# Performance work log

Measured on AMD Instinct MI355X. Metric: run time of the kernel, lower is better.

The kernel has to match this reference:

```python
import jax, jax.numpy as jnp
import numpy as np

N_GT, N_NODES, N_SPECIES, N_EDGES, D, L = 512, 399, 200, 397, 64, 2


def setup_inputs() -> dict:
    rng = np.random.default_rng(0)
    # Random recursive trees: parent of node i is uniform in [0, i).
    par = (rng.random((N_GT, N_NODES - 1)) * np.arange(1, N_NODES)).astype(np.int64)
    child = np.broadcast_to(np.arange(1, N_NODES), (N_GT, N_NODES - 1))
    off = (np.arange(N_GT, dtype=np.int64) * N_NODES)[:, None]
    c = (child + off).ravel()
    p = (par + off).ravel()
    # Both directions, as in the original [2, 2E_gt] convention.
    edge_index = np.stack([np.concatenate([c, p]), np.concatenate([p, c])])
    sp = np.full(N_NODES, -1, dtype=np.int64)
    sp[:N_SPECIES] = np.arange(N_SPECIES)
    sp_ids = np.tile(sp, N_GT)
    leaf_mask = sp_ids >= 0
    batch_vec = np.repeat(np.arange(N_GT, dtype=np.int64), N_NODES)
    # Clades: random species subsets per species-tree edge, guaranteed nonempty.
    pe = rng.uniform(0.05, 0.5, (N_EDGES, 1))
    clade_mask = rng.random((N_EDGES, N_SPECIES)) < pe
    clade_mask[np.arange(N_EDGES), rng.integers(0, N_SPECIES, N_EDGES)] = True
    key = jax.random.key(0)
    ks = jax.random.split(key, 3)
    s = 1.0 / np.sqrt(D)
    return {
        "edge_index": jnp.asarray(edge_index),
        "sp_ids": jnp.asarray(sp_ids),
        "leaf_mask": jnp.asarray(leaf_mask),
        "batch_vec": jnp.asarray(batch_vec),
        "clade_mask": jnp.asarray(clade_mask),
        "n_gt": N_GT,
        "emb_table": jax.random.normal(ks[0], (N_SPECIES + 1, D), jnp.float32),
        "W1": jax.random.normal(ks[1], (L, D, D), jnp.float32) * s,
        "b1": jnp.zeros((L, D), jnp.float32),
        "W2": jax.random.normal(ks[2], (L, D, D), jnp.float32) * s,
        "b2": jnp.zeros((L, D), jnp.float32),
        "eps": jnp.zeros((L,), jnp.float32),  # GINConv train_eps init 0
        "ln_gamma": jnp.ones((L, D), jnp.float32),
        "ln_beta": jnp.zeros((L, D), jnp.float32),
    }


def _layernorm(x, g, b):
    mu = x.mean(-1, keepdims=True)
    var = ((x - mu) ** 2).mean(-1, keepdims=True)
    return (x - mu) * jax.lax.rsqrt(var + 1e-5) * g + b


def reference(edge_index, sp_ids, leaf_mask, batch_vec, clade_mask, n_gt,
              emb_table, W1, b1, W2, b2, eps, ln_gamma, ln_beta):
    n_nodes = sp_ids.shape[0]
    n_edges, n_species = clade_mask.shape
    d = emb_table.shape[1]
    # Species embedding (internal nodes -> extra row n_species).
    emb_ids = jnp.where(sp_ids < 0, n_species, sp_ids)
    x = emb_table[emb_ids]  # [Nn, D]
    src, dst = edge_index[0], edge_index[1]
    for l in range(W1.shape[0]):
        # GINConv: mlp((1+eps)*x + sum_neighbors x_j), residual, LayerNorm.
        msg = jax.ops.segment_sum(x[src], dst, num_segments=n_nodes)
        h = (1.0 + eps[l]) * x + msg
        h = jax.nn.relu(h @ W1[l] + b1[l]) @ W2[l] + b2[l]
        x = _layernorm(x + h, ln_gamma[l], ln_beta[l])
        # dropout is identity in eval mode
    # Species pooling: mean over valid leaves per (gene tree, species).
    w = (leaf_mask & (sp_ids >= 0)).astype(x.dtype)  # [Nn]
    comp = batch_vec * n_species + jnp.maximum(sp_ids, 0)
    pool_size = n_gt * n_species
    sums = jax.ops.segment_sum(x * w[:, None], comp, num_segments=pool_size)
    cnts = jax.ops.segment_sum(w, comp, num_segments=pool_size)
    pool = (sums / jnp.maximum(cnts, 1.0)[:, None]).reshape(n_gt, n_species, d)
    valid = (cnts > 0).astype(x.dtype).reshape(n_gt, n_species)  # [G, S]
    # Clade pooling per species-tree edge (vectorized over the per-edge loop).
    mf = clade_mask.astype(x.dtype)  # [E, S]
    csum = jnp.einsum('es,gsd->egd', mf, pool * valid[:, :, None])  # [E,G,D]
    ccnt = mf @ valid.T  # [E, G] valid-species count per (edge, gene tree)
    gt_means = csum / jnp.maximum(ccnt, 1.0)[:, :, None]
    has = (ccnt > 0).astype(x.dtype)  # gene trees with data for this edge
    n_v = has.sum(1)  # [E]
    mean = (gt_means * has[:, :, None]).sum(1) / jnp.maximum(n_v, 1.0)[:, None]
    diff = (gt_means - mean[:, None, :]) * has[:, :, None]
    var = (diff ** 2).sum(1) / jnp.maximum(n_v - 1.0, 1.0)[:, None]  # unbiased
    ok = (n_v > 1)[:, None]
    std = jnp.where(ok, jnp.sqrt(jnp.where(ok, var, 1.0)), 0.0)
    mean = jnp.where((n_v > 0)[:, None], mean, 0.0)
    return jnp.concatenate([mean, std], axis=-1)  # [n_edges, 2*D]
```

## Files before the change

kernel.cpp:

```cpp
#include <hip/hip_runtime.h>

#define SMAX 200
#define NPG 399

typedef __bf16 bf16x8 __attribute__((ext_vector_type(8)));
typedef _Float16 half8 __attribute__((ext_vector_type(8)));
typedef float f32x4 __attribute__((ext_vector_type(4)));

__device__ __forceinline__ unsigned short f2bf(float f) {
  unsigned u = __float_as_uint(f);
  unsigned r = (u + 0x7FFFu + ((u >> 16) & 1u)) >> 16;
  return (unsigned short)r;
}
__device__ __forceinline__ int xel(int node, int dim) {
  return node * 64 + ((((dim >> 3)) ^ (node & 7)) << 3) + (dim & 7);
}

__global__ __launch_bounds__(256) void k_prep(const int* __restrict__ clade,
                                              unsigned short* __restrict__ mfA,
                                              unsigned* __restrict__ mfbits,
                                              int n_edges, int n_species) {
  int stride = gridDim.x * 256;
  for (int idx = blockIdx.x * 256 + threadIdx.x; idx < 25 * 7 * 512;
       idx += stride) {
    int fi = idx >> 9, within = idx & 511;
    int mt = fi / 7, kt = fi % 7;
    int l = within >> 3, j = within & 7;
    int e = mt * 16 + (l & 15);
    int s = kt * 32 + ((l >> 4) & 3) * 8 + j;
    unsigned short v = 0;
    if (e < n_edges && s < n_species && clade[(size_t)e * n_species + s] != 0)
      v = 0x3F80;
    mfA[idx] = v;
  }
  for (int idx = blockIdx.x * 256 + threadIdx.x; idx < 400 * 8; idx += stride) {
    int e = idx >> 3, w = idx & 7;
    unsigned bits = 0;
    if (e < n_edges && w < 7) {
      for (int b = 0; b < 32; ++b) {
        int s = w * 32 + b;
        if (s < n_species && clade[(size_t)e * n_species + s] != 0)
          bits |= 1u << b;
      }
    }
    mfbits[idx] = bits;
  }
}

__global__ __launch_bounds__(512) void k_tree(
    const float* __restrict__ emb, const int* __restrict__ sp,
    const int* __restrict__ leaf, const int* __restrict__ src,
    const int* __restrict__ dst, const float* __restrict__ W1,
    const float* __restrict__ b1, const float* __restrict__ W2,
    const float* __restrict__ b2, const float* __restrict__ eps_p,
    const float* __restrict__ gam, const float* __restrict__ bet,
    const unsigned short* __restrict__ mfA, const unsigned* __restrict__ mfbits,
    float* __restrict__ gmat, float* __restrict__ has, int npg, int n_species,
    int n_edges, int n_gt) {
  __shared__ __attribute__((aligned(16))) _Float16 sA[NPG * 64];
  __shared__ __attribute__((aligned(16))) _Float16 sB[NPG * 64];
  __shared__ __attribute__((aligned(16))) _Float16 sWf[2][2][4096];
  __shared__ __attribute__((aligned(16))) _Float16 sT[8][1024];
  __shared__ int sStart[NPG + 1];
  __shared__ int sChild[NPG - 1];
  __shared__ int sPar[NPG];
  __shared__ int sCnt[NPG];

  int g = blockIdx.x, tid = threadIdx.x;
  int base = g * npg, nEt = npg - 1, ebase = g * nEt;
  int w = tid >> 6, lane = tid & 63;
  int cc = lane & 15, gq = lane >> 4;

  for (int i = tid; i < npg + 1; i += 512) sStart[i] = 0;
  for (int i = tid; i < npg; i += 512) sCnt[i] = 0;
  __syncthreads();
  for (int idx = tid; idx < 4096; idx += 512) {
    int k = idx >> 6, n = idx & 63;
    int frag = (k >> 5) * 4 + (n >> 4);
    int ln = ((k >> 3) & 3) * 16 + (n & 15);
    int j = k & 7;
    int o = frag * 512 + ln * 8 + j;
    sWf[0][0][o] = (_Float16)W1[idx];
    sWf[0][1][o] = (_Float16)W2[idx];
    sWf[1][0][o] = (_Float16)W1[4096 + idx];
    sWf[1][1][o] = (_Float16)W2[4096 + idx];
  }
  for (int idx = tid; idx < npg * 8; idx += 512) {
    int node = idx >> 3, ch = idx & 7;
    int s = sp[base + node];
    int row = (s < 0) ? n_species : s;
    float4 v0 = reinterpret_cast<const float4*>(emb)[row * 16 + ch * 2];
    float4 v1 = reinterpret_cast<const float4*>(emb)[row * 16 + ch * 2 + 1];
    half8 h;
    h[0] = (_Float16)v0.x; h[1] = (_Float16)v0.y;
    h[2] = (_Float16)v0.z; h[3] = (_Float16)v0.w;
    h[4] = (_Float16)v1.x; h[5] = (_Float16)v1.y;
    h[6] = (_Float16)v1.z; h[7] = (_Float16)v1.w;
    *reinterpret_cast<half8*>(&sA[node * 64 + ((ch ^ (node & 7)) << 3)]) = h;
  }
  for (int i = tid; i < nEt; i += 512) {
    int c = src[ebase + i] - base;
    int p = dst[ebase + i] - base;
    sPar[c] = p;
    atomicAdd(&sStart[p + 1], 1);
  }
  __syncthreads();
  if (w == 0) {
    int run = 0;
    for (int chunk = 0; chunk * 64 < npg + 1; ++chunk) {
      int idx = chunk * 64 + lane;
      int v = (idx < npg + 1) ? sStart[idx] : 0;
      for (int off = 1; off < 64; off <<= 1) {
        int t2 = __shfl_up(v, off);
        if (lane >= off) v += t2;
      }
      v += run;
      if (idx < npg + 1) sStart[idx] = v;
      run = __shfl(v, 63);
    }
  }
  __syncthreads();
  for (int c = tid + 1; c < npg; c += 512) {
    int p = sPar[c];
    int pos = sStart[p] + atomicAdd(&sCnt[p], 1);
    sChild[pos] = c;
  }
  __syncthreads();

  _Float16* tb = sT[w];
  for (int l = 0; l < 2; ++l) {
    const _Float16* xin = l ? sB : sA;
    _Float16* xout = l ? sA : sB;
    const half8* xin8 = reinterpret_cast<const half8*>(xin);
    float e1 = 1.0f + eps_p[l];
    float b1v[4], b2v[4], gv[4], bv[4];
#pragma unroll
    for (int nt = 0; nt < 4; ++nt) {
      b1v[nt] = b1[l * 64 + cc + 16 * nt];
      b2v[nt] = b2[l * 64 + cc + 16 * nt];
      gv[nt] = gam[l * 64 + cc + 16 * nt];
      bv[nt] = bet[l * 64 + cc + 16 * nt];
    }
    const half8* B1 = reinterpret_cast<const half8*>(sWf[l][0]);
    const half8* B2 = reinterpret_cast<const half8*>(sWf[l][1]);
    for (int t = w; t < 25; t += 8) {
      int n0 = t * 16;
      int node = n0 + cc;
      bool vn = node < npg;
      int nd2 = vn ? node : 0;
      int j = vn ? sStart[nd2] : 0;
      int e = vn ? sStart[nd2 + 1] : 0;
      half8 s0 = xin8[nd2 * 8 + (gq ^ (nd2 & 7))];
      half8 s1 = xin8[nd2 * 8 + ((4 + gq) ^ (nd2 & 7))];
      bool hasp = vn && node > 0;
      int pr = hasp ? sPar[nd2] : 0;
      half8 p0 = xin8[pr * 8 + (gq ^ (pr & 7))];
      half8 p1 = xin8[pr * 8 + ((4 + gq) ^ (pr & 7))];
      float a0f[8], a1f[8];
#pragma unroll
      for (int d = 0; d < 8; ++d) {
        a0f[d] = e1 * (float)s0[d] + (hasp ? (float)p0[d] : 0.f);
        a1f[d] = e1 * (float)s1[d] + (hasp ? (float)p1[d] : 0.f);
      }
      while (__any(j < e)) {
        bool act = j < e;
        int c = act ? sChild[j] : 0;
        half8 v0 = xin8[c * 8 + (gq ^ (c & 7))];
        half8 v1 = xin8[c * 8 + ((4 + gq) ^ (c & 7))];
        if (act) {
#pragma unroll
          for (int d = 0; d < 8; ++d) {
            a0f[d] += (float)v0[d];
            a1f[d] += (float)v1[d];
          }
          ++j;
        }
      }
      half8 a0, a1;
#pragma unroll
      for (int d = 0; d < 8; ++d) {
        a0[d] = (_Float16)a0f[d];
        a1[d] = (_Float16)a1f[d];
      }
      f32x4 tacc[4];
#pragma unroll
      for (int nt = 0; nt < 4; ++nt) tacc[nt] = (f32x4){0.f, 0.f, 0.f, 0.f};
#pragma unroll
      for (int nt = 0; nt < 4; ++nt) {
        tacc[nt] = __builtin_amdgcn_mfma_f32_16x16x32_f16(
            a0, B1[nt * 64 + lane], tacc[nt], 0, 0, 0);
        tacc[nt] = __builtin_amdgcn_mfma_f32_16x16x32_f16(
            a1, B1[(4 + nt) * 64 + lane], tacc[nt], 0, 0, 0);
      }
#pragma unroll
      for (int nt = 0; nt < 4; ++nt)
#pragma unroll
        for (int r = 0; r < 4; ++r) {
          int m = gq * 4 + r;
          tb[m * 64 + ((cc + 16 * nt) ^ ((m & 7) << 3))] =
              (_Float16)fmaxf(tacc[nt][r] + b1v[nt], 0.f);
        }
      int sw = (cc & 7) << 3;
      half8 c0 =
          *reinterpret_cast<const half8*>(&tb[cc * 64 + ((gq * 8) ^ sw)]);
      half8 c1 =
          *reinterpret_cast<const half8*>(&tb[cc * 64 + ((32 + gq * 8) ^ sw)]);
      f32x4 hacc[4];
#pragma unroll
      for (int nt = 0; nt < 4; ++nt) hacc[nt] = (f32x4){0.f, 0.f, 0.f, 0.f};
#pragma unroll
      for (int nt = 0; nt < 4; ++nt) {
        hacc[nt] = __builtin_amdgcn_mfma_f32_16x16x32_f16(
            c0, B2[nt * 64 + lane], hacc[nt], 0, 0, 0);
        hacc[nt] = __builtin_amdgcn_mfma_f32_16x16x32_f16(
            c1, B2[(4 + nt) * 64 + lane], hacc[nt], 0, 0, 0);
      }
      float y[4][4];
#pragma unroll
      for (int r = 0; r < 4; ++r) {
        int nd3 = n0 + gq * 4 + r;
        bool v3 = nd3 < npg;
        int nds = v3 ? nd3 : 0;
#pragma unroll
        for (int nt = 0; nt < 4; ++nt) {
          float xv = (float)xin[xel(nds, cc + 16 * nt)];
          y[r][nt] = (v3 ? xv : 0.f) + hacc[nt][r] + b2v[nt];
        }
      }
#pragma unroll
      for (int r = 0; r < 4; ++r) {
        float s = y[r][0] + y[r][1] + y[r][2] + y[r][3];
        s += __shfl_xor(s, 1);
        s += __shfl_xor(s, 2);
        s += __shfl_xor(s, 4);
        s += __shfl_xor(s, 8);
        float mu = s * (1.f / 64.f);
        float d0 = y[r][0] - mu, d1 = y[r][1] - mu;
        float d2 = y[r][2] - mu, d3 = y[r][3] - mu;
        float v = d0 * d0 + d1 * d1 + d2 * d2 + d3 * d3;
        v += __shfl_xor(v, 1);
        v += __shfl_xor(v, 2);
        v += __shfl_xor(v, 4);
        v += __shfl_xor(v, 8);
        float iv = rsqrtf(v * (1.f / 64.f) + 1e-5f);
        int nd3 = n0 + gq * 4 + r;
        if (nd3 < npg) {
#pragma unroll
          for (int nt = 0; nt < 4; ++nt)
            xout[xel(nd3, cc + 16 * nt)] =
                (_Float16)((y[r][nt] - mu) * iv * gv[nt] + bv[nt]);
        }
      }
    }
    __syncthreads();
  }

  unsigned short* sBfU = reinterpret_cast<unsigned short*>(&sWf[0][0][0]);
  char* aux = reinterpret_cast<char*>(&sT[0][0]);
  float* sInv = reinterpret_cast<float*>(aux);
  float* sHas = reinterpret_cast<float*>(aux + 1600);
  unsigned* svb = reinterpret_cast<unsigned*>(aux + 3200);
  for (int i = tid; i < n_species + 1; i += 512) sStart[i] = 0;
  for (int i = tid; i < n_species; i += 512) sCnt[i] = 0;
  __syncthreads();
  for (int i = tid; i < npg; i += 512) {
    int s = sp[base + i];
    if (s >= 0 && leaf[base + i] != 0) atomicAdd(&sStart[s + 1], 1);
  }
  __syncthreads();
  if (w == 0) {
    int run = 0;
    for (int chunk = 0; chunk * 64 < n_species + 1; ++chunk) {
      int idx = chunk * 64 + lane;
      int v = (idx < n_species + 1) ? sStart[idx] : 0;
      for (int off = 1; off < 64; off <<= 1) {
        int t2 = __shfl_up(v, off);
        if (lane >= off) v += t2;
      }
      v += run;
      if (idx < n_species + 1) sStart[idx] = v;
      run = __shfl(v, 63);
    }
  }
  __syncthreads();
  for (int i = tid; i < npg; i += 512) {
    int s = sp[base + i];
    if (s >= 0 && leaf[base + i] != 0) {
      int pos = sStart[s] + atomicAdd(&sCnt[s], 1);
      sPar[pos] = i;
    }
  }
  __syncthreads();
  for (int idx = tid; idx < 14336; idx += 512) {
    int frag = idx >> 9;
    int ln = (idx >> 3) & 63;
    int jj = idx & 7;
    int s = (frag >> 2) * 32 + ((ln >> 4) & 3) * 8 + jj;
    int d = (frag & 3) * 16 + (ln & 15);
    float v = 0.f;
    if (s < n_species) {
      int j0 = sStart[s], j1 = sStart[s + 1];
      float sum = 0.f;
      for (int j2 = j0; j2 < j1; ++j2) {
        int nd4 = sPar[j2];
        sum += (float)sA[xel(nd4, d)];
      }
      if (j1 > j0) v = sum / (float)(j1 - j0);
    }
    sBfU[idx] = f2bf(v);
  }
  if (tid < 7) {
    unsigned bits = 0;
    for (int b = 0; b < 32; ++b) {
      int s = tid * 32 + b;
      if (s < n_species && sStart[s + 1] > sStart[s]) bits |= 1u << b;
    }
    svb[tid] = bits;
  }
  __syncthreads();
  for (int e = tid; e < 400; e += 512) {
    unsigned ccv = 0;
#pragma unroll
    for (int w2 = 0; w2 < 7; ++w2) ccv += __popc(mfbits[e * 8 + w2] & svb[w2]);
    sInv[e] = 1.f / (float)max(ccv, 1u);
    sHas[e] = (ccv > 0) ? 1.f : 0.f;
  }
  __syncthreads();
  const bf16x8* A = reinterpret_cast<const bf16x8*>(mfA);
  const bf16x8* Bb = reinterpret_cast<const bf16x8*>(sBfU);
  for (int mt = w; mt < 25; mt += 8) {
    bf16x8 af[7];
#pragma unroll
    for (int kt = 0; kt < 7; ++kt) af[kt] = A[(mt * 7 + kt) * 64 + lane];
    f32x4 acc0 = {0.f, 0.f, 0.f, 0.f};
    f32x4 acc1 = {0.f, 0.f, 0.f, 0.f};
    f32x4 acc2 = {0.f, 0.f, 0.f, 0.f};
    f32x4 acc3 = {0.f, 0.f, 0.f, 0.f};
#pragma unroll
    for (int kt = 0; kt < 7; ++kt) {
      const bf16x8* B = Bb + kt * 256 + lane;
      acc0 = __builtin_amdgcn_mfma_f32_16x16x32_bf16(af[kt], B[0], acc0, 0, 0, 0);
      acc1 = __builtin_amdgcn_mfma_f32_16x16x32_bf16(af[kt], B[64], acc1, 0, 0, 0);
      acc2 = __builtin_amdgcn_mfma_f32_16x16x32_bf16(af[kt], B[128], acc2, 0, 0, 0);
      acc3 = __builtin_amdgcn_mfma_f32_16x16x32_bf16(af[kt], B[192], acc3, 0, 0, 0);
    }
    int rbase = mt * 16 + (lane >> 4) * 4;
    int col = lane & 15;
#pragma unroll
    for (int r = 0; r < 4; ++r) {
      int e = rbase + r;
      if (e >= n_edges) continue;
      float inv = sInv[e];
      float* gp = gmat + ((size_t)e * n_gt + g) * 64 + col;
      gp[0] = acc0[r] * inv;
      gp[16] = acc1[r] * inv;
      gp[32] = acc2[r] * inv;
      gp[48] = acc3[r] * inv;
      if (col == 0) has[(size_t)e * n_gt + g] = sHas[e];
    }
  }
}

__global__ __launch_bounds__(512) void k_stat(const float* __restrict__ gmat,
                                              const float* __restrict__ has,
                                              float* __restrict__ out,
                                              int n_gt) {
  __shared__ float red1[8][64];
  __shared__ float red2[8][64];
  __shared__ float redn[8];
  int e = blockIdx.x;
  int tid = threadIdx.x, w = tid >> 6, lane = tid & 63;
  const float* ge = gmat + (size_t)e * n_gt * 64;
  const float* he = has + (size_t)e * n_gt;
  float S1 = 0.f, S2 = 0.f, nv = 0.f;
  for (int g = w; g < n_gt; g += 8) {
    float h = he[g];
    float v = ge[g * 64 + lane];
    S1 += h * v;
    S2 += h * v * v;
    nv += h;
  }
  red1[w][lane] = S1;
  red2[w][lane] = S2;
  if (lane == 0) redn[w] = nv;
  __syncthreads();
  if (w == 0) {
    float s1 = 0.f, s2 = 0.f, n_v = 0.f;
#pragma unroll
    for (int j = 0; j < 8; ++j) {
      s1 += red1[j][lane];
      s2 += red2[j][lane];
      n_v += redn[j];
    }
    float mean = s1 / fmaxf(n_v, 1.f);
    float var = (s2 - s1 * s1 / fmaxf(n_v, 1.f)) / fmaxf(n_v - 1.f, 1.f);
    float stdv = (n_v > 1.f) ? sqrtf(fmaxf(var, 0.f)) : 0.f;
    out[(size_t)e * 128 + lane] = (n_v > 0.f) ? mean : 0.f;
    out[(size_t)e * 128 + 64 + lane] = stdv;
  }
}

extern "C" void kernel_launch(void* const* d_in, const int* in_sizes, int n_in,
                              void* d_out, int out_size, void* d_ws, size_t ws_size,
                              hipStream_t stream) {
  (void)n_in; (void)out_size; (void)ws_size;
  const int* edge_index = (const int*)d_in[0];
  const int* sp_ids = (const int*)d_in[1];
  const int* leaf_mask = (const int*)d_in[2];
  const int* clade_mask = (const int*)d_in[4];
  const float* emb = (const float*)d_in[6];
  const float* W1 = (const float*)d_in[7];
  const float* b1 = (const float*)d_in[8];
  const float* W2 = (const float*)d_in[9];
  const float* b2 = (const float*)d_in[10];
  const float* eps = (const float*)d_in[11];
  const float* lng = (const float*)d_in[12];
  const float* lnb = (const float*)d_in[13];
  float* out = (float*)d_out;

  const int n_nodes = in_sizes[1];
  const int nE = in_sizes[0] / 2;
  const int n_species = in_sizes[6] / 64 - 1;
  const int n_edges = in_sizes[4] / n_species;
  const int n_gt = 512;
  const int npg = n_nodes / n_gt;

  const int* src = edge_index;
  const int* dst = edge_index + nE;

  float* gmat = (float*)d_ws;
  size_t gsz = ((size_t)n_edges * n_gt * 64 * sizeof(float) + 255ul) & ~255ul;
  float* has = (float*)((char*)d_ws + gsz);
  size_t hsz = ((size_t)n_edges * n_gt * sizeof(float) + 255ul) & ~255ul;
  unsigned short* mfA = (unsigned short*)((char*)d_ws + gsz + hsz);
  size_t masz = ((size_t)25 * 7 * 512 * sizeof(unsigned short) + 255ul) & ~255ul;
  unsigned* mfbits = (unsigned*)((char*)d_ws + gsz + hsz + masz);

  k_prep<<<64, 256, 0, stream>>>(clade_mask, mfA, mfbits, n_edges, n_species);
  k_tree<<<n_gt, 512, 0, stream>>>(emb, sp_ids, leaf_mask, src, dst, W1, b1,
                                   W2, b2, eps, lng, lnb, mfA, mfbits, gmat,
                                   has, npg, n_species, n_edges, n_gt);
  k_stat<<<n_edges, 512, 0, stream>>>(gmat, has, out, n_gt);
}
```

Before: 135.0 us.

## Store per-tree clade means in fp16 and restructure tree aggregation loops

The intermediate gmat buffer (edges x gene trees x 64) is now written and read as fp16 instead of fp32, halving the global traffic between k_tree and k_stat. The GIN neighbor loop now runs to a wave-uniform maximum child count instead of re-testing __any each step, and tiles are split into contiguous per-wave ranges. Species pooling now gathers 8 dims per thread with vector LDS loads instead of one scalar per thread, after zero-filling the bf16 buffer. The fp16 intermediate costs precision in the mean and std statistics, and the last wave takes four tiles while the others take three.

Result: faster. 123.0 us (-8.9%).

```diff
diff --git a/kernel.cpp b/kernel.cpp
--- a/kernel.cpp
+++ b/kernel.cpp
@@ -55,8 +55,8 @@
     const float* __restrict__ b2, const float* __restrict__ eps_p,
     const float* __restrict__ gam, const float* __restrict__ bet,
     const unsigned short* __restrict__ mfA, const unsigned* __restrict__ mfbits,
-    float* __restrict__ gmat, float* __restrict__ has, int npg, int n_species,
-    int n_edges, int n_gt) {
+    _Float16* __restrict__ gmat, float* __restrict__ has, int npg,
+    int n_species, int n_edges, int n_gt) {
   __shared__ __attribute__((aligned(16))) _Float16 sA[NPG * 64];
   __shared__ __attribute__((aligned(16))) _Float16 sB[NPG * 64];
   __shared__ __attribute__((aligned(16))) _Float16 sWf[2][2][4096];
@@ -128,6 +128,8 @@
   __syncthreads();
 
   _Float16* tb = sT[w];
+  int t0w = w * 3;
+  int t1w = (w == 7) ? 25 : t0w + 3;
   for (int l = 0; l < 2; ++l) {
     const _Float16* xin = l ? sB : sA;
     _Float16* xout = l ? sA : sB;
@@ -143,13 +145,13 @@
     }
     const half8* B1 = reinterpret_cast<const half8*>(sWf[l][0]);
     const half8* B2 = reinterpret_cast<const half8*>(sWf[l][1]);
-    for (int t = w; t < 25; t += 8) {
+    for (int t = t0w; t < t1w; ++t) {
       int n0 = t * 16;
       int node = n0 + cc;
       bool vn = node < npg;
       int nd2 = vn ? node : 0;
-      int j = vn ? sStart[nd2] : 0;
-      int e = vn ? sStart[nd2 + 1] : 0;
+      int j0v = vn ? sStart[nd2] : 0;
+      int cnt = vn ? (sStart[nd2 + 1] - j0v) : 0;
       half8 s0 = xin8[nd2 * 8 + (gq ^ (nd2 & 7))];
       half8 s1 = xin8[nd2 * 8 + ((4 + gq) ^ (nd2 & 7))];
       bool hasp = vn && node > 0;
@@ -162,9 +164,16 @@
         a0f[d] = e1 * (float)s0[d] + (hasp ? (float)p0[d] : 0.f);
         a1f[d] = e1 * (float)s1[d] + (hasp ? (float)p1[d] : 0.f);
       }
-      while (__any(j < e)) {
-        bool act = j < e;
-        int c = act ? sChild[j] : 0;
+      int cmax = cnt;
+#pragma unroll
+      for (int off = 1; off < 64; off <<= 1)
+        cmax = max(cmax, __shfl_xor(cmax, off));
+      cmax = __builtin_amdgcn_readfirstlane(cmax);
+#pragma unroll 2
+      for (int k = 0; k < cmax; ++k) {
+        bool act = k < cnt;
+        int jidx = act ? (j0v + k) : 0;
+        int c = sChild[jidx];
         half8 v0 = xin8[c * 8 + (gq ^ (c & 7))];
         half8 v1 = xin8[c * 8 + ((4 + gq) ^ (c & 7))];
         if (act) {
@@ -173,7 +182,6 @@
             a0f[d] += (float)v0[d];
             a1f[d] += (float)v1[d];
           }
-          ++j;
         }
       }
       half8 a0, a1;
@@ -262,6 +270,11 @@
   unsigned* svb = reinterpret_cast<unsigned*>(aux + 3200);
   for (int i = tid; i < n_species + 1; i += 512) sStart[i] = 0;
   for (int i = tid; i < n_species; i += 512) sCnt[i] = 0;
+  {
+    float4 z4 = {0.f, 0.f, 0.f, 0.f};
+    for (int i = tid; i < 1792; i += 512)
+      reinterpret_cast<float4*>(sBfU)[i] = z4;
+  }
   __syncthreads();
   for (int i = tid; i < npg; i += 512) {
     int s = sp[base + i];
@@ -291,23 +304,25 @@
     }
   }
   __syncthreads();
-  for (int idx = tid; idx < 14336; idx += 512) {
-    int frag = idx >> 9;
-    int ln = (idx >> 3) & 63;
-    int jj = idx & 7;
-    int s = (frag >> 2) * 32 + ((ln >> 4) & 3) * 8 + jj;
-    int d = (frag & 3) * 16 + (ln & 15);
-    float v = 0.f;
-    if (s < n_species) {
-      int j0 = sStart[s], j1 = sStart[s + 1];
-      float sum = 0.f;
-      for (int j2 = j0; j2 < j1; ++j2) {
-        int nd4 = sPar[j2];
-        sum += (float)sA[xel(nd4, d)];
-      }
-      if (j1 > j0) v = sum / (float)(j1 - j0);
-    }
-    sBfU[idx] = f2bf(v);
+  for (int idx = tid; idx < n_species * 8; idx += 512) {
+    int s = idx >> 3, dc = idx & 7;
+    int j0 = sStart[s], j1 = sStart[s + 1];
+    float sum[8] = {0.f, 0.f, 0.f, 0.f, 0.f, 0.f, 0.f, 0.f};
+    for (int j2 = j0; j2 < j1; ++j2) {
+      int nd = sPar[j2];
+      half8 v = *reinterpret_cast<const half8*>(
+          &sA[nd * 64 + ((dc ^ (nd & 7)) << 3)]);
+#pragma unroll
+      for (int dd = 0; dd < 8; ++dd) sum[dd] += (float)v[dd];
+    }
+    float invc = (j1 > j0) ? 1.f / (float)(j1 - j0) : 0.f;
+#pragma unroll
+    for (int dd = 0; dd < 8; ++dd) {
+      int d = dc * 8 + dd;
+      int frag = (s >> 5) * 4 + (d >> 4);
+      int ln = ((s >> 3) & 3) * 16 + (d & 15);
+      sBfU[frag * 512 + ln * 8 + (s & 7)] = f2bf(sum[dd] * invc);
+    }
   }
   if (tid < 7) {
     unsigned bits = 0;
@@ -351,17 +366,17 @@
       int e = rbase + r;
       if (e >= n_edges) continue;
       float inv = sInv[e];
-      float* gp = gmat + ((size_t)e * n_gt + g) * 64 + col;
-      gp[0] = acc0[r] * inv;
-      gp[16] = acc1[r] * inv;
-      gp[32] = acc2[r] * inv;
-      gp[48] = acc3[r] * inv;
+      _Float16* gp = gmat + ((size_t)e * n_gt + g) * 64 + col;
+      gp[0] = (_Float16)(acc0[r] * inv);
+      gp[16] = (_Float16)(acc1[r] * inv);
+      gp[32] = (_Float16)(acc2[r] * inv);
+      gp[48] = (_Float16)(acc3[r] * inv);
       if (col == 0) has[(size_t)e * n_gt + g] = sHas[e];
     }
   }
 }
 
-__global__ __launch_bounds__(512) void k_stat(const float* __restrict__ gmat,
+__global__ __launch_bounds__(512) void k_stat(const _Float16* __restrict__ gmat,
                                               const float* __restrict__ has,
                                               float* __restrict__ out,
                                               int n_gt) {
@@ -370,12 +385,12 @@
   __shared__ float redn[8];
   int e = blockIdx.x;
   int tid = threadIdx.x, w = tid >> 6, lane = tid & 63;
-  const float* ge = gmat + (size_t)e * n_gt * 64;
+  const _Float16* ge = gmat + (size_t)e * n_gt * 64;
   const float* he = has + (size_t)e * n_gt;
   float S1 = 0.f, S2 = 0.f, nv = 0.f;
   for (int g = w; g < n_gt; g += 8) {
     float h = he[g];
-    float v = ge[g * 64 + lane];
+    float v = (float)ge[g * 64 + lane];
     S1 += h * v;
     S2 += h * v * v;
     nv += h;
@@ -428,8 +443,9 @@
   const int* src = edge_index;
   const int* dst = edge_index + nE;
 
-  float* gmat = (float*)d_ws;
-  size_t gsz = ((size_t)n_edges * n_gt * 64 * sizeof(float) + 255ul) & ~255ul;
+  _Float16* gmat = (_Float16*)d_ws;
+  size_t gsz =
+      ((size_t)n_edges * n_gt * 64 * sizeof(_Float16) + 255ul) & ~255ul;
   float* has = (float*)((char*)d_ws + gsz);
   size_t hsz = ((size_t)n_edges * n_gt * sizeof(float) + 255ul) & ~255ul;
   unsigned short* mfA = (unsigned short*)((char*)d_ws + gsz + hsz);
```
